# Kernel optimization log

Measured on AMD Instinct MI355X. Metric: run time of the kernel, lower is better.

The kernel has to match this reference:

```python
import jax, jax.numpy as jnp
import numpy as np

N_NODES = 10000
N_EDGES = 160000
N_FEAT = 128      # n_features
N_BASIS = 20      # n_basis
N_LAYERS = 3      # n_interactions
N_GRAPHS = 64
CUTOFF = 5.0
VOCAB = 119       # 118 elements + padding idx 0


def setup_inputs() -> dict:
    key = jax.random.key(0)
    ks = jax.random.split(key, 20)
    z = jax.random.randint(ks[0], (N_NODES,), 0, VOCAB)
    pos = jax.random.normal(ks[1], (N_NODES, 3), dtype=jnp.float32) * 2.0
    cell = jax.random.normal(ks[2], (N_GRAPHS, 3, 3), dtype=jnp.float32)
    batch = jnp.sort(jax.random.randint(ks[3], (N_NODES,), 0, N_GRAPHS))
    edge_index = jax.random.randint(ks[4], (2, N_EDGES), 0, N_NODES)

    s = 1.0 / np.sqrt(N_FEAT)
    node_emb = jax.random.normal(ks[5], (VOCAB, N_FEAT), dtype=jnp.float32) * 0.1
    node_emb = node_emb.at[0].set(0.0)  # padding_idx=0
    # per-layer stacked parameters (L, ...)
    mnp_W1 = jax.random.normal(ks[6], (N_LAYERS, N_FEAT, N_FEAT), dtype=jnp.float32) * s
    mnp_b1 = jnp.zeros((N_LAYERS, N_FEAT), dtype=jnp.float32)
    mnp_W2 = jax.random.normal(ks[7], (N_LAYERS, N_FEAT, N_FEAT), dtype=jnp.float32) * s
    mnp_b2 = jnp.zeros((N_LAYERS, N_FEAT), dtype=jnp.float32)
    me_W = jax.random.normal(ks[8], (N_LAYERS, N_BASIS, N_FEAT), dtype=jnp.float32) * (1.0 / np.sqrt(N_BASIS))
    em1_W1 = jax.random.normal(ks[9], (N_LAYERS, N_FEAT, N_FEAT), dtype=jnp.float32) * s
    em1_W2 = jax.random.normal(ks[10], (N_LAYERS, N_FEAT, N_FEAT), dtype=jnp.float32) * s
    em2_W1 = jax.random.normal(ks[11], (N_LAYERS, N_FEAT, N_FEAT), dtype=jnp.float32) * s
    em2_W2 = jax.random.normal(ks[12], (N_LAYERS, N_FEAT, N_FEAT), dtype=jnp.float32) * s
    eu_W = jax.random.normal(ks[13], (N_LAYERS, N_FEAT, N_FEAT), dtype=jnp.float32) * s
    return {
        "z": z, "pos": pos, "cell": cell, "batch": batch, "edge_index": edge_index,
        "node_emb": node_emb,
        "mnp_W1": mnp_W1, "mnp_b1": mnp_b1, "mnp_W2": mnp_W2, "mnp_b2": mnp_b2,
        "me_W": me_W, "em1_W1": em1_W1, "em1_W2": em1_W2,
        "em2_W1": em2_W1, "em2_W2": em2_W2, "eu_W": eu_W,
    }


def _edge_embedding(pos_d, edge_index):
    """Gaussian RBF x cosine cutoff; dir = unit displacement vectors."""
    i, j = edge_index[0], edge_index[1]
    diff = pos_d[j] - pos_d[i]                      # (E, 3)
    d = jnp.sqrt(jnp.sum(diff * diff, axis=-1) + 1e-12)  # (E,)
    dir_edge = diff / d[:, None]                    # (E, 3)
    centers = jnp.linspace(0.0, CUTOFF, N_BASIS)
    width = CUTOFF / N_BASIS
    rbf = jnp.exp(-jnp.square((d[:, None] - centers) / width))  # (E, B)
    fc = 0.5 * (jnp.cos(jnp.pi * d / CUTOFF) + 1.0) * (d < CUTOFF)
    return rbf * fc[:, None], dir_edge


def reference(z, pos, cell, batch, edge_index, node_emb,
              mnp_W1, mnp_b1, mnp_W2, mnp_b2, me_W,
              em1_W1, em1_W2, em2_W1, em2_W2, eu_W):
    n = z.shape[0]
    atom = node_emb[z]                                   # (N, F)
    force = jnp.zeros((n, 3, N_FEAT), dtype=pos.dtype)   # (N, 3, F)

    # strain displacement bookkeeping (identity in plain forward)
    disp = jnp.broadcast_to(jnp.eye(3, dtype=pos.dtype), cell.shape)  # (G,3,3)
    sym = 0.5 * (disp + jnp.swapaxes(disp, -1, -2))
    pos_d = jnp.einsum('nd,nde->ne', pos, sym[batch])

    dist_edge, dir_edge = _edge_embedding(pos_d, edge_index)
    i, j = edge_index[0], edge_index[1]

    for l in range(N_LAYERS):
        # invariant node/edge message parts
        h = jax.nn.silu(atom @ mnp_W1[l] + mnp_b1[l]) @ mnp_W2[l] + mnp_b2[l]  # (N,F)
        me = dist_edge @ me_W[l]                                               # (E,F)
        msg = me * h[i] * h[j]                                                 # (E,F)
        atom = atom + jax.ops.segment_sum(msg, i, num_segments=n)
        # equivariant messages
        e1 = (jax.nn.silu(msg @ em1_W1[l]) @ em1_W2[l])[:, None, :] * dir_edge[:, :, None]  # (E,3,F)
        e2 = (jax.nn.silu(msg @ em2_W1[l]) @ em2_W2[l])[:, None, :] * force[j]              # (E,3,F)
        force = force + jax.ops.segment_sum(e1 + e2, i, num_segments=n)
        atom = atom + jnp.sum(force * (force @ eu_W[l]), axis=1)
    return atom, force
```

## Files before the change

### kernel.cpp

```cpp
#include <hip/hip_runtime.h>
#include <hip/hip_bf16.h>
#include <math.h>

#define NN 10000
#define NE 160000
#define NF 128
#define NB 20
#define CUT 5.0f
#define TPS 136
#define TPF 132

typedef __attribute__((ext_vector_type(8))) short short8;
typedef __attribute__((ext_vector_type(4))) float floatx4;
typedef unsigned short u16;
typedef unsigned int u32;

__device__ __forceinline__ u16 f2b(float x){
  union { __hip_bfloat16 b; u16 u; } cv;
  cv.b = __float2bfloat16(x);
  return cv.u;
}
__device__ __forceinline__ float lo_bf(u32 w){ return __uint_as_float(w << 16); }
__device__ __forceinline__ float hi_bf(u32 w){ return __uint_as_float(w & 0xFFFF0000u); }
__device__ __forceinline__ u32 packbf(float lo, float hi){
  return ((u32)f2b(hi) << 16) | (u32)f2b(lo);
}
__device__ __forceinline__ float fast_silu(float v){
  return v * __builtin_amdgcn_rcpf(1.f + __expf(-v));
}
__device__ __forceinline__ float rdf(const void* p, size_t i, int isb){
  return isb ? __bfloat162float(((const __hip_bfloat16*)p)[i]) : ((const float*)p)[i];
}

__global__ __launch_bounds__(256) void k_detect(const void* __restrict__ w, int nelem,
                                                int* __restrict__ flag){
  __shared__ int cnt;
  if (threadIdx.x == 0) cnt = 0;
  __syncthreads();
  const u16* hw = (const u16*)w;
  int local = 0;
  for (int k = threadIdx.x; k < nelem; k += 256){
    u16 h = hw[k];
    int e = (h >> 7) & 0xFF;
    if ((h & 0x7FFF) == 0 || (e >= 103 && e <= 130)) local++;
  }
  atomicAdd(&cnt, local);
  __syncthreads();
  if (threadIdx.x == 0) *flag = (cnt >= (nelem * 9) / 10) ? 1 : 0;
}

struct PrepArgs {
  const void* csrc[4]; float* cdst[4]; int cn[4];
  const void* ssrc[7]; u16* sdst[7];
  const void* mesrc;   u16* medst;
};
__global__ __launch_bounds__(256) void k_prep(PrepArgs a, const int* __restrict__ flag){
  int y = blockIdx.y;
  int isb = *flag;
  if (y < 4){
    const void* s = a.csrc[y]; float* d = a.cdst[y]; int n = a.cn[y];
    for (int i = blockIdx.x*256 + threadIdx.x; i < n; i += gridDim.x*256)
      d[i] = rdf(s, i, isb);
  } else if (y < 11){
    const void* s = a.ssrc[y-4]; u16* d = a.sdst[y-4];
    int idx = blockIdx.x*256 + threadIdx.x;
    int l = idx >> 14, rem = idx & 16383;
    int j = rem & 7, lane = (rem >> 3) & 63, tn = (rem >> 9) & 7, tk = rem >> 12;
    int k = tk*32 + ((lane >> 4) & 3)*8 + j, n = tn*16 + (lane & 15);
    d[idx] = f2b(rdf(s, (size_t)l*16384 + k*NF + n, isb));
  } else {
    int idx = blockIdx.x*256 + threadIdx.x;
    if (idx >= 3*4096) return;
    int l = idx >> 12, rem = idx & 4095;
    int j = rem & 7, lane = (rem >> 3) & 63, tn = rem >> 9;
    int k = ((lane >> 4) & 3)*8 + j, n = tn*16 + (lane & 15);
    a.medst[idx] = (k < NB) ? f2b(rdf(a.mesrc, (size_t)l*NB*NF + k*NF + n, isb)) : (u16)0;
  }
}

__global__ __launch_bounds__(256) void k_hist(const int* __restrict__ ei, int* __restrict__ count){
  int e = blockIdx.x*256 + threadIdx.x;
  if (e < NE) atomicAdd(&count[ei[e]], 1);
}
__global__ __launch_bounds__(256) void k_scan(const int* __restrict__ count,
                                              int* __restrict__ rowptr, int* __restrict__ cursor){
  __shared__ int part[256];
  const int CH = (NN + 255) / 256;
  int t = threadIdx.x;
  int base = t * CH;
  int s = 0;
  for (int k = 0; k < CH; k++){ int i = base + k; if (i < NN) s += count[i]; }
  part[t] = s;
  __syncthreads();
  for (int off = 1; off < 256; off <<= 1){
    int v = (t >= off) ? part[t - off] : 0;
    __syncthreads();
    part[t] += v;
    __syncthreads();
  }
  int run = (t == 0) ? 0 : part[t - 1];
  for (int k = 0; k < CH; k++){
    int i = base + k;
    if (i < NN){ rowptr[i] = run; cursor[i] = run; run += count[i]; }
  }
  if (t == 255) rowptr[NN] = run;
}
__global__ __launch_bounds__(256) void k_scatter_embed(const int* __restrict__ ei,
                                                       int* __restrict__ cursor,
                                                       const float* __restrict__ pos,
                                                       int* __restrict__ iis, int* __restrict__ jjs,
                                                       float* __restrict__ ds, float* __restrict__ dirs){
  int e = blockIdx.x * 256 + threadIdx.x;
  if (e >= NE) return;
  int i = ei[e], j = ei[NE + e];
  float dx = pos[j*3+0] - pos[i*3+0];
  float dy = pos[j*3+1] - pos[i*3+1];
  float dz = pos[j*3+2] - pos[i*3+2];
  float d = sqrtf(dx*dx + dy*dy + dz*dz + 1e-12f);
  float inv = 1.0f / d;
  int s = atomicAdd(&cursor[i], 1);
  iis[s] = i; jjs[s] = j;
  ds[s] = d;
  dirs[s*3+0] = dx*inv; dirs[s*3+1] = dy*inv; dirs[s*3+2] = dz*inv;
}

__global__ __launch_bounds__(64, 4) void k_mlp0(
    const int* __restrict__ z, const float* __restrict__ emb,
    float* __restrict__ atom,
    const u16* __restrict__ w1sw, const float* __restrict__ b1,
    const u16* __restrict__ w2sw, const float* __restrict__ b2,
    u32* __restrict__ hb)
{
  __shared__ __align__(16) u16 tileT[16][TPS];
  const int lane = threadIdx.x;
  const int q = lane >> 4, ln = lane & 15;
  const int n0 = blockIdx.x * 16;
  const int zn = z[n0 + ln];

  floatx4 c1[8];
  #pragma unroll
  for (int tn = 0; tn < 8; tn++) c1[tn] = (floatx4){0,0,0,0};
  #pragma unroll
  for (int tk = 0; tk < 4; tk++){
    const float4 u0 = *(const float4*)&emb[(size_t)zn*NF + tk*32 + q*8];
    const float4 u1 = *(const float4*)&emb[(size_t)zn*NF + tk*32 + q*8 + 4];
    *(float4*)&atom[(size_t)(n0+ln)*NF + tk*32 + q*8]     = u0;
    *(float4*)&atom[(size_t)(n0+ln)*NF + tk*32 + q*8 + 4] = u1;
    short8 a;
    a[0]=(short)f2b(u0.x); a[1]=(short)f2b(u0.y); a[2]=(short)f2b(u0.z); a[3]=(short)f2b(u0.w);
    a[4]=(short)f2b(u1.x); a[5]=(short)f2b(u1.y); a[6]=(short)f2b(u1.z); a[7]=(short)f2b(u1.w);
    #pragma unroll
    for (int tn = 0; tn < 8; tn++){
      short8 b = *(const short8*)(w1sw + (size_t)((tk*8 + tn)*64 + lane)*8);
      c1[tn] = __builtin_amdgcn_mfma_f32_16x16x32_bf16(a, b, c1[tn], 0, 0, 0);
    }
  }
  #pragma unroll
  for (int tn = 0; tn < 8; tn++){
    int n = tn*16 + ln;
    float bias = b1[n];
    #pragma unroll
    for (int r = 0; r < 4; r++)
      tileT[q*4 + r][n] = f2b(fast_silu(c1[tn][r] + bias));
  }
  floatx4 c2[8];
  #pragma unroll
  for (int tn = 0; tn < 8; tn++) c2[tn] = (floatx4){0,0,0,0};
  #pragma unroll
  for (int tk = 0; tk < 4; tk++){
    short8 a = *(const short8*)&tileT[ln][tk*32 + q*8];
    #pragma unroll
    for (int tn = 0; tn < 8; tn++){
      short8 b = *(const short8*)(w2sw + (size_t)((tk*8 + tn)*64 + lane)*8);
      c2[tn] = __builtin_amdgcn_mfma_f32_16x16x32_bf16(a, b, c2[tn], 0, 0, 0);
    }
  }
  float b2n[8];
  #pragma unroll
  for (int tn = 0; tn < 8; tn++) b2n[tn] = b2[tn*16 + ln];
  #pragma unroll
  for (int tn = 0; tn < 4; tn++){
    #pragma unroll
    for (int r = 0; r < 4; r++){
      float vl = c2[tn][r]   + b2n[tn];
      float vh = c2[tn+4][r] + b2n[tn+4];
      hb[(size_t)(n0 + q*4 + r)*64 + tn*16 + ln] = packbf(vl, vh);
    }
  }
}

#define SEGFLUSH(ADDR_EXPR)                                               \
  {                                                                       \
    float s0_ = 0.f, s1_ = 0.f;                                           \
    _Pragma("unroll")                                                     \
    for (int m_ = 0; m_ < 16; m_++){                                      \
      float2 w_ = *(const float2*)&tileF[wv][m_][c0];                     \
      s0_ += w_.x; s1_ += w_.y;                                           \
      if (m_ == 15 || ((bmask >> (m_ + 1)) & 1u)){                        \
        int ii_ = __builtin_amdgcn_readlane(curii, m_);                   \
        float* p_ = (ADDR_EXPR);                                          \
        atomicAdd(p_ + c0,     s0_);                                      \
        atomicAdd(p_ + c0 + 1, s1_);                                      \
        s0_ = 0.f; s1_ = 0.f;                                             \
      }                                                                   \
    }                                                                     \
  }

__global__ __launch_bounds__(128, 2) void k_edge_mfma(
    const int* __restrict__ iis, const int* __restrict__ jjs,
    const float* __restrict__ ds, const float* __restrict__ dirs,
    const u32* __restrict__ hb,
    const u16* __restrict__ mesw,
    const u16* __restrict__ w11sw, const u16* __restrict__ w12sw,
    const u16* __restrict__ w21sw, const u16* __restrict__ w22sw,
    float* __restrict__ atom, const u32* __restrict__ forceb, float* __restrict__ fdelta)
{
  __shared__ __align__(16) u16 tileM[2][16][TPS];
  __shared__ __align__(16) float tileF[2][16][TPF];

  const int wv = threadIdx.x >> 6;
  const int lane = threadIdx.x & 63;
  const int q = lane >> 4, ln = lane & 15;
  const int bid = (blockIdx.x & 7) * (gridDim.x >> 3) + (blockIdx.x >> 3);
  const int e0 = (bid*2 + wv) * 16;
  const int c0 = lane * 2;

  const int l16 = lane & 15;
  int curii = iis[e0 + l16];
  int previi = (l16 == 0) ? ~curii : iis[e0 + l16 - 1];
  const u32 bmask = (u32)__ballot(lane < 16 && (curii != previi));

  int iiR[4], jjR[4];
  float dirR[4][3];
  #pragma unroll
  for (int r = 0; r < 4; r++){
    int s = e0 + q*4 + r;
    iiR[r] = iis[s]; jjR[r] = jjs[s];
    dirR[r][0] = dirs[s*3+0]; dirR[r][1] = dirs[s*3+1]; dirR[r][2] = dirs[s*3+2];
  }

  u32 hiw[4][4], hjw[4][4];
  #pragma unroll
  for (int r = 0; r < 4; r++)
    #pragma unroll
    for (int t4 = 0; t4 < 4; t4++){
      hiw[r][t4] = hb[(size_t)iiR[r]*64 + t4*16 + ln];
      hjw[r][t4] = hb[(size_t)jjR[r]*64 + t4*16 + ln];
    }

  float dA  = ds[e0 + ln];
  float fcA = (dA < CUT) ? 0.5f*(cosf((float)M_PI*dA*(1.0f/CUT)) + 1.0f) : 0.0f;
  short8 a_rbf;
  #pragma unroll
  for (int j = 0; j < 8; j++){
    int k = q*8 + j;
    float v = 0.f;
    if (k < NB){
      float t = (dA - CUT*(float)k/(float)(NB-1)) * ((float)NB/CUT);
      v = __expf(-t*t) * fcA;
    }
    a_rbf[j] = (short)f2b(v);
  }

  #pragma unroll
  for (int tn = 0; tn < 8; tn++){
    short8 b = *(const short8*)(mesw + (size_t)(tn*64 + lane)*8);
    floatx4 c = {0.f,0.f,0.f,0.f};
    c = __builtin_amdgcn_mfma_f32_16x16x32_bf16(a_rbf, b, c, 0, 0, 0);
    int n = tn*16 + ln;
    int t4 = tn & 3;
    #pragma unroll
    for (int r = 0; r < 4; r++){
      float hi_ = (tn < 4) ? lo_bf(hiw[r][t4]) : hi_bf(hiw[r][t4]);
      float hj_ = (tn < 4) ? lo_bf(hjw[r][t4]) : hi_bf(hjw[r][t4]);
      float mv = c[r] * hi_ * hj_;
      tileF[wv][q*4 + r][n] = mv;
      tileM[wv][q*4 + r][n] = f2b(mv);
    }
  }

  SEGFLUSH(&atom[(size_t)ii_ * NF])

  floatx4 c2[8], c1[8];
  #pragma unroll
  for (int tn = 0; tn < 8; tn++){ c2[tn] = (floatx4){0,0,0,0}; c1[tn] = (floatx4){0,0,0,0}; }
  #pragma unroll
  for (int tk = 0; tk < 4; tk++){
    short8 a = *(const short8*)&tileM[wv][ln][tk*32 + q*8];
    #pragma unroll
    for (int tn = 0; tn < 8; tn++){
      short8 b2 = *(const short8*)(w21sw + (size_t)((tk*8 + tn)*64 + lane)*8);
      c2[tn] = __builtin_amdgcn_mfma_f32_16x16x32_bf16(a, b2, c2[tn], 0, 0, 0);
      short8 b1 = *(const short8*)(w11sw + (size_t)((tk*8 + tn)*64 + lane)*8);
      c1[tn] = __builtin_amdgcn_mfma_f32_16x16x32_bf16(a, b1, c1[tn], 0, 0, 0);
    }
  }
  #pragma unroll
  for (int tn = 0; tn < 8; tn++){
    int n = tn*16 + ln;
    #pragma unroll
    for (int r = 0; r < 4; r++){
      tileM[wv][q*4 + r][n] = f2b(fast_silu(c1[tn][r]));
      c2[tn][r] = fast_silu(c2[tn][r]);
    }
  }

  floatx4 g1[8];
  #pragma unroll
  for (int tn = 0; tn < 8; tn++) g1[tn] = (floatx4){0,0,0,0};
  #pragma unroll
  for (int tk = 0; tk < 4; tk++){
    short8 a = *(const short8*)&tileM[wv][ln][tk*32 + q*8];
    #pragma unroll
    for (int tn = 0; tn < 8; tn++){
      short8 b = *(const short8*)(w12sw + (size_t)((tk*8 + tn)*64 + lane)*8);
      g1[tn] = __builtin_amdgcn_mfma_f32_16x16x32_bf16(a, b, g1[tn], 0, 0, 0);
    }
  }
  #pragma unroll
  for (int tn = 0; tn < 8; tn++){
    int n = tn*16 + ln;
    #pragma unroll
    for (int r = 0; r < 4; r++) tileM[wv][q*4 + r][n] = f2b(c2[tn][r]);
  }
  #pragma unroll
  for (int tn = 0; tn < 8; tn++) c1[tn] = (floatx4){0,0,0,0};
  #pragma unroll
  for (int tk = 0; tk < 4; tk++){
    short8 a = *(const short8*)&tileM[wv][ln][tk*32 + q*8];
    #pragma unroll
    for (int tn = 0; tn < 8; tn++){
      short8 b = *(const short8*)(w22sw + (size_t)((tk*8 + tn)*64 + lane)*8);
      c1[tn] = __builtin_amdgcn_mfma_f32_16x16x32_bf16(a, b, c1[tn], 0, 0, 0);
    }
  }

  for (int d = 0; d < 3; d++){
    u32 fjw[4][4];
    #pragma unroll
    for (int r = 0; r < 4; r++)
      #pragma unroll
      for (int t4 = 0; t4 < 4; t4++)
        fjw[r][t4] = forceb[((size_t)jjR[r]*3 + d)*64 + t4*16 + ln];
    #pragma unroll
    for (int tn = 0; tn < 8; tn++){
      int n = tn*16 + ln;
      int t4 = tn & 3;
      #pragma unroll
      for (int r = 0; r < 4; r++){
        float fj = (tn < 4) ? lo_bf(fjw[r][t4]) : hi_bf(fjw[r][t4]);
        tileF[wv][q*4 + r][n] = g1[tn][r]*dirR[r][d] + c1[tn][r]*fj;
      }
    }
    SEGFLUSH(&fdelta[((size_t)ii_*3 + d)*NF])
  }
}

__global__ __launch_bounds__(64, 4) void k_node_upd(
    float* __restrict__ force, float* __restrict__ fdelta,
    const u16* __restrict__ eusw, u32* __restrict__ forceb,
    float* __restrict__ saccp)
{
  __shared__ __align__(16) u16 tile[16][TPS];
  __shared__ __align__(16) float tileF[16][TPF];
  const int lane = threadIdx.x;
  const int q = lane >> 4, ln = lane & 15;
  const int n0 = blockIdx.x * 16;
  const int d  = blockIdx.y;

  #pragma unroll
  for (int m = 0; m < 16; m++){
    size_t idx = ((size_t)(n0+m)*3 + d)*NF + lane;
    float v0 = force[idx]    + fdelta[idx];
    float v1 = force[idx+64] + fdelta[idx+64];
    force[idx] = v0; force[idx+64] = v1;
    fdelta[idx] = 0.f; fdelta[idx+64] = 0.f;
    forceb[((size_t)(n0+m)*3 + d)*64 + lane] = packbf(v0, v1);
    tile[m][lane]    = f2b(v0);
    tile[m][lane+64] = f2b(v1);
    tileF[m][lane]    = v0;
    tileF[m][lane+64] = v1;
  }
  floatx4 c[8];
  #pragma unroll
  for (int tn = 0; tn < 8; tn++) c[tn] = (floatx4){0,0,0,0};
  #pragma unroll
  for (int tk = 0; tk < 4; tk++){
    short8 a = *(const short8*)&tile[ln][tk*32 + q*8];
    #pragma unroll
    for (int tn = 0; tn < 8; tn++){
      short8 b = *(const short8*)(eusw + (size_t)((tk*8 + tn)*64 + lane)*8);
      c[tn] = __builtin_amdgcn_mfma_f32_16x16x32_bf16(a, b, c[tn], 0, 0, 0);
    }
  }
  #pragma unroll
  for (int tn = 0; tn < 8; tn++){
    int n = tn*16 + ln;
    #pragma unroll
    for (int r = 0; r < 4; r++)
      saccp[((size_t)d*NN + n0 + q*4 + r)*NF + n] = tileF[q*4 + r][n] * c[tn][r];
  }
}

__global__ __launch_bounds__(64, 2) void k_node_mlpB(
    const float* __restrict__ saccp, float* __restrict__ atom,
    const u16* __restrict__ w1sw, const float* __restrict__ b1,
    const u16* __restrict__ w2sw, const float* __restrict__ b2,
    u32* __restrict__ hb, int do_mlp)
{
  __shared__ __align__(16) u16 tile[16][TPS];
  const int lane = threadIdx.x;
  const int q = lane >> 4, ln = lane & 15;
  const int n0 = blockIdx.x * 16;

  float anew[8][4];
  #pragma unroll
  for (int tn = 0; tn < 8; tn++){
    int n = tn*16 + ln;
    #pragma unroll
    for (int r = 0; r < 4; r++){
      size_t p = ((size_t)(n0 + q*4 + r))*NF + n;
      float s = saccp[p] + saccp[(size_t)NN*NF + p] + saccp[(size_t)2*NN*NF + p];
      size_t idx = (size_t)(n0 + q*4 + r)*NF + n;
      float v = atom[idx] + s;
      atom[idx] = v;
      anew[tn][r] = v;
    }
  }
  if (!do_mlp) return;

  #pragma unroll
  for (int tn = 0; tn < 8; tn++){
    int n = tn*16 + ln;
    #pragma unroll
    for (int r = 0; r < 4; r++) tile[q*4 + r][n] = f2b(anew[tn][r]);
  }
  floatx4 c1[8];
  #pragma unroll
  for (int tn = 0; tn < 8; tn++) c1[tn] = (floatx4){0,0,0,0};
  #pragma unroll
  for (int tk = 0; tk < 4; tk++){
    short8 a = *(const short8*)&tile[ln][tk*32 + q*8];
    #pragma unroll
    for (int tn = 0; tn < 8; tn++){
      short8 b = *(const short8*)(w1sw + (size_t)((tk*8 + tn)*64 + lane)*8);
      c1[tn] = __builtin_amdgcn_mfma_f32_16x16x32_bf16(a, b, c1[tn], 0, 0, 0);
    }
  }
  #pragma unroll
  for (int tn = 0; tn < 8; tn++){
    int n = tn*16 + ln;
    float bias = b1[n];
    #pragma unroll
    for (int r = 0; r < 4; r++)
      tile[q*4 + r][n] = f2b(fast_silu(c1[tn][r] + bias));
  }
  floatx4 c2[8];
  #pragma unroll
  for (int tn = 0; tn < 8; tn++) c2[tn] = (floatx4){0,0,0,0};
  #pragma unroll
  for (int tk = 0; tk < 4; tk++){
    short8 a = *(const short8*)&tile[ln][tk*32 + q*8];
    #pragma unroll
    for (int tn = 0; tn < 8; tn++){
      short8 b = *(const short8*)(w2sw + (size_t)((tk*8 + tn)*64 + lane)*8);
      c2[tn] = __builtin_amdgcn_mfma_f32_16x16x32_bf16(a, b, c2[tn], 0, 0, 0);
    }
  }
  float b2n[8];
  #pragma unroll
  for (int tn = 0; tn < 8; tn++) b2n[tn] = b2[tn*16 + ln];
  #pragma unroll
  for (int tn = 0; tn < 4; tn++){
    #pragma unroll
    for (int r = 0; r < 4; r++){
      float vl = c2[tn][r]   + b2n[tn];
      float vh = c2[tn+4][r] + b2n[tn+4];
      hb[(size_t)(n0 + q*4 + r)*64 + tn*16 + ln] = packbf(vl, vh);
    }
  }
}

__global__ __launch_bounds__(256) void k_writeout(const float* __restrict__ atom,
                                                  const float* __restrict__ force,
                                                  void* __restrict__ out,
                                                  const int* __restrict__ flag){
  int idx = blockIdx.x * 256 + threadIdx.x;
  const int na = NN * NF;
  const int tot = na + NN * 3 * NF;
  if (idx >= tot) return;
  float v = (idx < na) ? atom[idx] : force[idx - na];
  if (*flag) ((__hip_bfloat16*)out)[idx] = __float2bfloat16(v);
  else       ((float*)out)[idx] = v;
}

extern "C" void kernel_launch(void* const* d_in, const int* in_sizes, int n_in,
                              void* d_out, int out_size, void* d_ws, size_t ws_size,
                              hipStream_t stream){
  const int* z    = (const int*)d_in[0];
  const void* pos = d_in[1];
  const int* ei   = (const int*)d_in[4];
  const void* emb   = d_in[5];
  const void* mnpW1 = d_in[6];
  const void* mnpb1 = d_in[7];
  const void* mnpW2 = d_in[8];
  const void* mnpb2 = d_in[9];
  const void* meW   = d_in[10];
  const void* em1W1 = d_in[11];
  const void* em1W2 = d_in[12];
  const void* em2W1 = d_in[13];
  const void* em2W2 = d_in[14];
  const void* euW   = d_in[15];

  float* base  = (float*)d_ws;
  int*   flag  = (int*)d_ws;
  float* atom   = base + 4;
  float* force  = atom   + NN*NF;
  float* fdelta = force  + (size_t)NN*3*NF;
  u32*   forceb = (u32*)(fdelta + (size_t)NN*3*NF);
  int*   count  = (int*)(forceb + (size_t)NN*3*64);
  float* ds    = (float*)(count + NN);
  float* dirs  = ds + NE;
  float* posf  = dirs + 3*NE;
  float* embf  = posf + NN*3;
  float* b1f   = embf + 119*NF;
  float* b2f_  = b1f + 3*NF;
  u32*   hb    = (u32*)(b2f_ + 3*NF);
  u16*   mesw  = (u16*)(hb + (size_t)NN*64);
  u16*   w11sw = mesw  + 3*4096;
  u16*   w12sw = w11sw + 3*16384;
  u16*   w21sw = w12sw + 3*16384;
  u16*   w22sw = w21sw + 3*16384;
  u16*   w1sw  = w22sw + 3*16384;
  u16*   w2sw  = w1sw  + 3*16384;
  u16*   eusw  = w2sw  + 3*16384;
  int* rowptr  = (int*)(eusw + 3*16384);
  int* cursor  = rowptr + NN + 1;
  int* iis     = cursor + NN;
  int* jjs     = iis + NE;
  float* saccp = (float*)(jjs + NE);

  k_detect<<<1, 256, 0, stream>>>(meW, 3*NB*NF, flag);

  hipMemsetAsync(force, 0, ((size_t)NN*3*NF*2 + (size_t)NN*3*64 + NN)*4, stream);

  PrepArgs pa;
  pa.csrc[0]=pos;   pa.cdst[0]=posf; pa.cn[0]=NN*3;
  pa.csrc[1]=emb;   pa.cdst[1]=embf; pa.cn[1]=119*NF;
  pa.csrc[2]=mnpb1; pa.cdst[2]=b1f;  pa.cn[2]=3*NF;
  pa.csrc[3]=mnpb2; pa.cdst[3]=b2f_; pa.cn[3]=3*NF;
  pa.ssrc[0]=em1W1; pa.sdst[0]=w11sw;
  pa.ssrc[1]=em1W2; pa.sdst[1]=w12sw;
  pa.ssrc[2]=em2W1; pa.sdst[2]=w21sw;
  pa.ssrc[3]=em2W2; pa.sdst[3]=w22sw;
  pa.ssrc[4]=mnpW1; pa.sdst[4]=w1sw;
  pa.ssrc[5]=mnpW2; pa.sdst[5]=w2sw;
  pa.ssrc[6]=euW;   pa.sdst[6]=eusw;
  pa.mesrc=meW;     pa.medst=mesw;
  k_prep<<<dim3(192,12), 256, 0, stream>>>(pa, flag);

  k_hist         <<<(NE+255)/256, 256, 0, stream>>>(ei, count);
  k_scan         <<<1, 256, 0, stream>>>(count, rowptr, cursor);
  k_scatter_embed<<<(NE+255)/256, 256, 0, stream>>>(ei, cursor, posf, iis, jjs, ds, dirs);

  k_mlp0<<<NN/16, 64, 0, stream>>>(z, embf, atom, w1sw, b1f, w2sw, b2f_, hb);
  for (int l = 0; l < 3; l++){
    k_edge_mfma<<<NE/32, 128, 0, stream>>>(iis, jjs, ds, dirs, hb,
        mesw  + (size_t)l*4096,
        w11sw + (size_t)l*16384, w12sw + (size_t)l*16384,
        w21sw + (size_t)l*16384, w22sw + (size_t)l*16384,
        atom, forceb, fdelta);
    k_node_upd<<<dim3(NN/16, 3), 64, 0, stream>>>(force, fdelta,
        eusw + (size_t)l*16384, forceb, saccp);
    int nl = l + 1;
    k_node_mlpB<<<NN/16, 64, 0, stream>>>(saccp, atom,
        w1sw + (size_t)(nl%3)*16384, b1f + (size_t)(nl%3)*NF,
        w2sw + (size_t)(nl%3)*16384, b2f_ + (size_t)(nl%3)*NF,
        hb, (l < 2) ? 1 : 0);
  }

  k_writeout<<<(NN*NF + NN*3*NF + 255)/256, 256, 0, stream>>>(atom, force, d_out, flag);
}
```

Measured before the change: 590.3 us.

## Split edge tile columns across waves and fuse node force update with MLP

The edge kernel now has both waves of a block work on the same 16-edge tile, each owning half of the 128 output columns. This halves the per-wave accumulator arrays and lets launch bounds allow 4 blocks per SM, at the cost of block-level barriers and twice as many blocks. Separately, the per-direction force-update kernel and the atom MLP kernel are merged into one kernel that loops over the three directions and accumulates in registers. That removes the saccp scratch buffer round trip and one launch per layer, but cuts node-stage parallelism threefold.

```diff
diff --git a/kernel.cpp b/kernel.cpp
--- a/kernel.cpp
+++ b/kernel.cpp
@@ -191,22 +191,20 @@
 
 #define SEGFLUSH(ADDR_EXPR)                                               \
   {                                                                       \
-    float s0_ = 0.f, s1_ = 0.f;                                           \
+    float s_ = 0.f;                                                       \
     _Pragma("unroll")                                                     \
     for (int m_ = 0; m_ < 16; m_++){                                      \
-      float2 w_ = *(const float2*)&tileF[wv][m_][c0];                     \
-      s0_ += w_.x; s1_ += w_.y;                                           \
+      s_ += tileF[m_][cc];                                                \
       if (m_ == 15 || ((bmask >> (m_ + 1)) & 1u)){                        \
         int ii_ = __builtin_amdgcn_readlane(curii, m_);                   \
         float* p_ = (ADDR_EXPR);                                          \
-        atomicAdd(p_ + c0,     s0_);                                      \
-        atomicAdd(p_ + c0 + 1, s1_);                                      \
-        s0_ = 0.f; s1_ = 0.f;                                             \
+        atomicAdd(p_ + cc, s_);                                           \
+        s_ = 0.f;                                                         \
       }                                                                   \
     }                                                                     \
   }
 
-__global__ __launch_bounds__(128, 2) void k_edge_mfma(
+__global__ __launch_bounds__(128, 4) void k_edge_mfma(
     const int* __restrict__ iis, const int* __restrict__ jjs,
     const float* __restrict__ ds, const float* __restrict__ dirs,
     const u32* __restrict__ hb,
@@ -215,15 +213,16 @@
     const u16* __restrict__ w21sw, const u16* __restrict__ w22sw,
     float* __restrict__ atom, const u32* __restrict__ forceb, float* __restrict__ fdelta)
 {
-  __shared__ __align__(16) u16 tileM[2][16][TPS];
-  __shared__ __align__(16) float tileF[2][16][TPF];
+  __shared__ __align__(16) u16 tileM[16][TPS];
+  __shared__ __align__(16) float tileF[16][TPF];
+  u16* tileFu = (u16*)&tileF[0][0];
 
   const int wv = threadIdx.x >> 6;
   const int lane = threadIdx.x & 63;
   const int q = lane >> 4, ln = lane & 15;
   const int bid = (blockIdx.x & 7) * (gridDim.x >> 3) + (blockIdx.x >> 3);
-  const int e0 = (bid*2 + wv) * 16;
-  const int c0 = lane * 2;
+  const int e0 = bid * 16;
+  const int cc = wv*64 + lane;
 
   const int l16 = lane & 15;
   int curii = iis[e0 + l16];
@@ -243,9 +242,9 @@
   #pragma unroll
   for (int r = 0; r < 4; r++)
     #pragma unroll
-    for (int t4 = 0; t4 < 4; t4++){
-      hiw[r][t4] = hb[(size_t)iiR[r]*64 + t4*16 + ln];
-      hjw[r][t4] = hb[(size_t)jjR[r]*64 + t4*16 + ln];
+    for (int t = 0; t < 4; t++){
+      hiw[r][t] = hb[(size_t)iiR[r]*64 + t*16 + ln];
+      hjw[r][t] = hb[(size_t)jjR[r]*64 + t*16 + ln];
     }
 
   float dA  = ds[e0 + ln];
@@ -263,75 +262,84 @@
   }
 
   #pragma unroll
-  for (int tn = 0; tn < 8; tn++){
-    short8 b = *(const short8*)(mesw + (size_t)(tn*64 + lane)*8);
+  for (int t = 0; t < 4; t++){
+    const int tn_g = wv*4 + t;
+    short8 b = *(const short8*)(mesw + (size_t)(tn_g*64 + lane)*8);
     floatx4 c = {0.f,0.f,0.f,0.f};
     c = __builtin_amdgcn_mfma_f32_16x16x32_bf16(a_rbf, b, c, 0, 0, 0);
-    int n = tn*16 + ln;
-    int t4 = tn & 3;
+    const int n = tn_g*16 + ln;
     #pragma unroll
     for (int r = 0; r < 4; r++){
-      float hi_ = (tn < 4) ? lo_bf(hiw[r][t4]) : hi_bf(hiw[r][t4]);
-      float hj_ = (tn < 4) ? lo_bf(hjw[r][t4]) : hi_bf(hjw[r][t4]);
+      float hi_ = wv ? hi_bf(hiw[r][t]) : lo_bf(hiw[r][t]);
+      float hj_ = wv ? hi_bf(hjw[r][t]) : lo_bf(hjw[r][t]);
       float mv = c[r] * hi_ * hj_;
-      tileF[wv][q*4 + r][n] = mv;
-      tileM[wv][q*4 + r][n] = f2b(mv);
+      tileF[q*4 + r][n] = mv;
+      tileM[q*4 + r][n] = f2b(mv);
     }
   }
 
   SEGFLUSH(&atom[(size_t)ii_ * NF])
 
-  floatx4 c2[8], c1[8];
-  #pragma unroll
-  for (int tn = 0; tn < 8; tn++){ c2[tn] = (floatx4){0,0,0,0}; c1[tn] = (floatx4){0,0,0,0}; }
-  #pragma unroll
-  for (int tk = 0; tk < 4; tk++){
-    short8 a = *(const short8*)&tileM[wv][ln][tk*32 + q*8];
-    #pragma unroll
-    for (int tn = 0; tn < 8; tn++){
-      short8 b2 = *(const short8*)(w21sw + (size_t)((tk*8 + tn)*64 + lane)*8);
-      c2[tn] = __builtin_amdgcn_mfma_f32_16x16x32_bf16(a, b2, c2[tn], 0, 0, 0);
-      short8 b1 = *(const short8*)(w11sw + (size_t)((tk*8 + tn)*64 + lane)*8);
-      c1[tn] = __builtin_amdgcn_mfma_f32_16x16x32_bf16(a, b1, c1[tn], 0, 0, 0);
-    }
-  }
-  #pragma unroll
-  for (int tn = 0; tn < 8; tn++){
-    int n = tn*16 + ln;
+  __syncthreads();
+
+  floatx4 c2[4], c1[4];
+  #pragma unroll
+  for (int t = 0; t < 4; t++){ c2[t] = (floatx4){0,0,0,0}; c1[t] = (floatx4){0,0,0,0}; }
+  #pragma unroll
+  for (int tk = 0; tk < 4; tk++){
+    short8 a = *(const short8*)&tileM[ln][tk*32 + q*8];
+    #pragma unroll
+    for (int t = 0; t < 4; t++){
+      const int tn_g = wv*4 + t;
+      short8 b2 = *(const short8*)(w21sw + (size_t)((tk*8 + tn_g)*64 + lane)*8);
+      c2[t] = __builtin_amdgcn_mfma_f32_16x16x32_bf16(a, b2, c2[t], 0, 0, 0);
+      short8 b1 = *(const short8*)(w11sw + (size_t)((tk*8 + tn_g)*64 + lane)*8);
+      c1[t] = __builtin_amdgcn_mfma_f32_16x16x32_bf16(a, b1, c1[t], 0, 0, 0);
+    }
+  }
+  #pragma unroll
+  for (int t = 0; t < 4; t++){
+    const int n = (wv*4 + t)*16 + ln;
     #pragma unroll
     for (int r = 0; r < 4; r++){
-      tileM[wv][q*4 + r][n] = f2b(fast_silu(c1[tn][r]));
-      c2[tn][r] = fast_silu(c2[tn][r]);
-    }
-  }
-
-  floatx4 g1[8];
-  #pragma unroll
-  for (int tn = 0; tn < 8; tn++) g1[tn] = (floatx4){0,0,0,0};
-  #pragma unroll
-  for (int tk = 0; tk < 4; tk++){
-    short8 a = *(const short8*)&tileM[wv][ln][tk*32 + q*8];
-    #pragma unroll
-    for (int tn = 0; tn < 8; tn++){
-      short8 b = *(const short8*)(w12sw + (size_t)((tk*8 + tn)*64 + lane)*8);
-      g1[tn] = __builtin_amdgcn_mfma_f32_16x16x32_bf16(a, b, g1[tn], 0, 0, 0);
-    }
-  }
-  #pragma unroll
-  for (int tn = 0; tn < 8; tn++){
-    int n = tn*16 + ln;
-    #pragma unroll
-    for (int r = 0; r < 4; r++) tileM[wv][q*4 + r][n] = f2b(c2[tn][r]);
-  }
-  #pragma unroll
-  for (int tn = 0; tn < 8; tn++) c1[tn] = (floatx4){0,0,0,0};
-  #pragma unroll
-  for (int tk = 0; tk < 4; tk++){
-    short8 a = *(const short8*)&tileM[wv][ln][tk*32 + q*8];
-    #pragma unroll
-    for (int tn = 0; tn < 8; tn++){
-      short8 b = *(const short8*)(w22sw + (size_t)((tk*8 + tn)*64 + lane)*8);
-      c1[tn] = __builtin_amdgcn_mfma_f32_16x16x32_bf16(a, b, c1[tn], 0, 0, 0);
+      tileFu[(q*4 + r)*TPS + n] = f2b(fast_silu(c1[t][r]));
+      c2[t][r] = fast_silu(c2[t][r]);
+    }
+  }
+
+  __syncthreads();
+
+  floatx4 g1[4];
+  #pragma unroll
+  for (int t = 0; t < 4; t++) g1[t] = (floatx4){0,0,0,0};
+  #pragma unroll
+  for (int tk = 0; tk < 4; tk++){
+    short8 a = *(const short8*)&tileFu[(size_t)ln*TPS + tk*32 + q*8];
+    #pragma unroll
+    for (int t = 0; t < 4; t++){
+      short8 b = *(const short8*)(w12sw + (size_t)((tk*8 + wv*4 + t)*64 + lane)*8);
+      g1[t] = __builtin_amdgcn_mfma_f32_16x16x32_bf16(a, b, g1[t], 0, 0, 0);
+    }
+  }
+  #pragma unroll
+  for (int t = 0; t < 4; t++){
+    const int n = (wv*4 + t)*16 + ln;
+    #pragma unroll
+    for (int r = 0; r < 4; r++) tileM[q*4 + r][n] = f2b(c2[t][r]);
+  }
+
+  __syncthreads();
+
+  floatx4 g2[4];
+  #pragma unroll
+  for (int t = 0; t < 4; t++) g2[t] = (floatx4){0,0,0,0};
+  #pragma unroll
+  for (int tk = 0; tk < 4; tk++){
+    short8 a = *(const short8*)&tileM[ln][tk*32 + q*8];
+    #pragma unroll
+    for (int t = 0; t < 4; t++){
+      short8 b = *(const short8*)(w22sw + (size_t)((tk*8 + wv*4 + t)*64 + lane)*8);
+      g2[t] = __builtin_amdgcn_mfma_f32_16x16x32_bf16(a, b, g2[t], 0, 0, 0);
     }
   }
 
@@ -340,89 +348,84 @@
     #pragma unroll
     for (int r = 0; r < 4; r++)
       #pragma unroll
-      for (int t4 = 0; t4 < 4; t4++)
-        fjw[r][t4] = forceb[((size_t)jjR[r]*3 + d)*64 + t4*16 + ln];
-    #pragma unroll
-    for (int tn = 0; tn < 8; tn++){
-      int n = tn*16 + ln;
-      int t4 = tn & 3;
+      for (int t = 0; t < 4; t++)
+        fjw[r][t] = forceb[((size_t)jjR[r]*3 + d)*64 + t*16 + ln];
+    #pragma unroll
+    for (int t = 0; t < 4; t++){
+      const int n = (wv*4 + t)*16 + ln;
       #pragma unroll
       for (int r = 0; r < 4; r++){
-        float fj = (tn < 4) ? lo_bf(fjw[r][t4]) : hi_bf(fjw[r][t4]);
-        tileF[wv][q*4 + r][n] = g1[tn][r]*dirR[r][d] + c1[tn][r]*fj;
+        float fj = wv ? hi_bf(fjw[r][t]) : lo_bf(fjw[r][t]);
+        tileF[q*4 + r][n] = g1[t][r]*dirR[r][d] + g2[t][r]*fj;
       }
     }
     SEGFLUSH(&fdelta[((size_t)ii_*3 + d)*NF])
   }
 }
 
-__global__ __launch_bounds__(64, 4) void k_node_upd(
+__global__ __launch_bounds__(64, 2) void k_node(
     float* __restrict__ force, float* __restrict__ fdelta,
     const u16* __restrict__ eusw, u32* __restrict__ forceb,
-    float* __restrict__ saccp)
+    float* __restrict__ atom,
+    const u16* __restrict__ w1sw, const float* __restrict__ b1,
+    const u16* __restrict__ w2sw, const float* __restrict__ b2,
+    u32* __restrict__ hb, int do_mlp)
 {
   __shared__ __align__(16) u16 tile[16][TPS];
   __shared__ __align__(16) float tileF[16][TPF];
   const int lane = threadIdx.x;
   const int q = lane >> 4, ln = lane & 15;
   const int n0 = blockIdx.x * 16;
-  const int d  = blockIdx.y;
-
-  #pragma unroll
-  for (int m = 0; m < 16; m++){
-    size_t idx = ((size_t)(n0+m)*3 + d)*NF + lane;
-    float v0 = force[idx]    + fdelta[idx];
-    float v1 = force[idx+64] + fdelta[idx+64];
-    force[idx] = v0; force[idx+64] = v1;
-    fdelta[idx] = 0.f; fdelta[idx+64] = 0.f;
-    forceb[((size_t)(n0+m)*3 + d)*64 + lane] = packbf(v0, v1);
-    tile[m][lane]    = f2b(v0);
-    tile[m][lane+64] = f2b(v1);
-    tileF[m][lane]    = v0;
-    tileF[m][lane+64] = v1;
-  }
-  floatx4 c[8];
-  #pragma unroll
-  for (int tn = 0; tn < 8; tn++) c[tn] = (floatx4){0,0,0,0};
-  #pragma unroll
-  for (int tk = 0; tk < 4; tk++){
-    short8 a = *(const short8*)&tile[ln][tk*32 + q*8];
+
+  float acc[8][4];
+  #pragma unroll
+  for (int tn = 0; tn < 8; tn++)
+    #pragma unroll
+    for (int r = 0; r < 4; r++) acc[tn][r] = 0.f;
+
+  for (int d = 0; d < 3; d++){
+    #pragma unroll
+    for (int m = 0; m < 16; m++){
+      size_t idx = ((size_t)(n0+m)*3 + d)*NF + lane;
+      float v0 = force[idx]    + fdelta[idx];
+      float v1 = force[idx+64] + fdelta[idx+64];
+      force[idx] = v0; force[idx+64] = v1;
+      fdelta[idx] = 0.f; fdelta[idx+64] = 0.f;
+      forceb[((size_t)(n0+m)*3 + d)*64 + lane] = packbf(v0, v1);
+      tile[m][lane]    = f2b(v0);
+      tile[m][lane+64] = f2b(v1);
+      tileF[m][lane]    = v0;
+      tileF[m][lane+64] = v1;
+    }
+    floatx4 c[8];
+    #pragma unroll
+    for (int tn = 0; tn < 8; tn++) c[tn] = (floatx4){0,0,0,0};
+    #pragma unroll
+    for (int tk = 0; tk < 4; tk++){
+      short8 a = *(const short8*)&tile[ln][tk*32 + q*8];
+      #pragma unroll
+      for (int tn = 0; tn < 8; tn++){
+        short8 b = *(const short8*)(eusw + (size_t)((tk*8 + tn)*64 + lane)*8);
+        c[tn] = __builtin_amdgcn_mfma_f32_16x16x32_bf16(a, b, c[tn], 0, 0, 0);
+      }
+    }
     #pragma unroll
     for (int tn = 0; tn < 8; tn++){
-      short8 b = *(const short8*)(eusw + (size_t)((tk*8 + tn)*64 + lane)*8);
-      c[tn] = __builtin_amdgcn_mfma_f32_16x16x32_bf16(a, b, c[tn], 0, 0, 0);
-    }
-  }
+      int n = tn*16 + ln;
+      #pragma unroll
+      for (int r = 0; r < 4; r++)
+        acc[tn][r] += tileF[q*4 + r][n] * c[tn][r];
+    }
+  }
+
+  float anew[8][4];
   #pragma unroll
   for (int tn = 0; tn < 8; tn++){
     int n = tn*16 + ln;
     #pragma unroll
-    for (int r = 0; r < 4; r++)
-      saccp[((size_t)d*NN + n0 + q*4 + r)*NF + n] = tileF[q*4 + r][n] * c[tn][r];
-  }
-}
-
-__global__ __launch_bounds__(64, 2) void k_node_mlpB(
-    const float* __restrict__ saccp, float* __restrict__ atom,
-    const u16* __restrict__ w1sw, const float* __restrict__ b1,
-    const u16* __restrict__ w2sw, const float* __restrict__ b2,
-    u32* __restrict__ hb, int do_mlp)
-{
-  __shared__ __align__(16) u16 tile[16][TPS];
-  const int lane = threadIdx.x;
-  const int q = lane >> 4, ln = lane & 15;
-  const int n0 = blockIdx.x * 16;
-
-  float anew[8][4];
-  #pragma unroll
-  for (int tn = 0; tn < 8; tn++){
-    int n = tn*16 + ln;
-    #pragma unroll
     for (int r = 0; r < 4; r++){
-      size_t p = ((size_t)(n0 + q*4 + r))*NF + n;
-      float s = saccp[p] + saccp[(size_t)NN*NF + p] + saccp[(size_t)2*NN*NF + p];
       size_t idx = (size_t)(n0 + q*4 + r)*NF + n;
-      float v = atom[idx] + s;
+      float v = atom[idx] + acc[tn][r];
       atom[idx] = v;
       anew[tn][r] = v;
     }
@@ -538,7 +541,6 @@
   int* cursor  = rowptr + NN + 1;
   int* iis     = cursor + NN;
   int* jjs     = iis + NE;
-  float* saccp = (float*)(jjs + NE);
 
   k_detect<<<1, 256, 0, stream>>>(meW, 3*NB*NF, flag);
 
@@ -565,15 +567,14 @@
 
   k_mlp0<<<NN/16, 64, 0, stream>>>(z, embf, atom, w1sw, b1f, w2sw, b2f_, hb);
   for (int l = 0; l < 3; l++){
-    k_edge_mfma<<<NE/32, 128, 0, stream>>>(iis, jjs, ds, dirs, hb,
+    k_edge_mfma<<<NE/16, 128, 0, stream>>>(iis, jjs, ds, dirs, hb,
         mesw  + (size_t)l*4096,
         w11sw + (size_t)l*16384, w12sw + (size_t)l*16384,
         w21sw + (size_t)l*16384, w22sw + (size_t)l*16384,
         atom, forceb, fdelta);
-    k_node_upd<<<dim3(NN/16, 3), 64, 0, stream>>>(force, fdelta,
-        eusw + (size_t)l*16384, forceb, saccp);
     int nl = l + 1;
-    k_node_mlpB<<<NN/16, 64, 0, stream>>>(saccp, atom,
+    k_node<<<NN/16, 64, 0, stream>>>(force, fdelta,
+        eusw + (size_t)l*16384, forceb, atom,
         w1sw + (size_t)(nl%3)*16384, b1f + (size_t)(nl%3)*NF,
         w2sw + (size_t)(nl%3)*16384, b2f_ + (size_t)(nl%3)*NF,
         hb, (l < 2) ? 1 : 0);
```

Result: faster. 561.1 us (-5.0%).
